# Optimization experiments

Hardware: AMD Instinct MI355X
Metric: run time of the kernel (lower is better)

The kernel has to match this reference:

```python
import jax, jax.numpy as jnp
import numpy as np


def _gru(x, Wih, Whh, bih, bhh):
    """Single-layer torch-style GRU, batch_first. x:[B,T,E], Wih:[3H,E], Whh:[3H,H]."""
    gi = jnp.einsum('bte,ge->btg', x, Wih) + bih  # precompute input gates [B,T,3H]
    H = Whh.shape[1]
    h0 = jnp.zeros((x.shape[0], H), x.dtype)

    def step(h, gi_t):
        gh = h @ Whh.T + bhh
        i_r, i_z, i_n = jnp.split(gi_t, 3, axis=-1)
        h_r, h_z, h_n = jnp.split(gh, 3, axis=-1)
        r = jax.nn.sigmoid(i_r + h_r)
        z = jax.nn.sigmoid(i_z + h_z)
        n = jnp.tanh(i_n + r * h_n)
        h_new = (1.0 - z) * n + z * h
        return h_new, h_new

    _, hs = jax.lax.scan(step, h0, jnp.swapaxes(gi, 0, 1))
    return jnp.swapaxes(hs, 0, 1)  # [B,T,H]


def setup_inputs() -> dict:
    V, E, H, B, S, Tc, Ts = 100000, 256, 256, 256, 10, 20, 50
    Bc = B * S
    k = jax.random.split(jax.random.key(0), 16)
    w = lambda kk, shp, s=0.05: (jax.random.normal(kk, shp) * s).astype(jnp.float32)
    return {
        'input_cate_batch': jax.random.randint(k[0], (Bc, Tc), 0, V),
        'mask_cate_batch': jnp.ones((Bc, Tc), jnp.float32),
        'mask_cate_seq_batch': jnp.ones((B, S), jnp.float32),
        'max_actionNum_cate_batch': Tc,
        'max_subseqNum_cate_batch': S,
        'subseqLen_cate_batch': jax.random.randint(k[1], (Bc,), 0, Tc),
        'seqLen_cate_batch': jax.random.randint(k[2], (B,), 0, S),
        'input_batch': jax.random.randint(k[3], (B, Ts), 0, V),
        'mask_batch': jnp.ones((B, Ts), jnp.float32),
        'seqLen_batch': jax.random.randint(k[4], (B,), 0, Ts),
        'target_y_batch': jax.random.randint(k[5], (B,), 0, V),
        'train_test_flag': 0,
        'emb': w(k[6], (V, E), 0.02),
        'Wih_c': w(k[7], (3 * H, E)), 'Whh_c': w(k[8], (3 * H, H)),
        'bih_c': jnp.zeros((3 * H,), jnp.float32), 'bhh_c': jnp.zeros((3 * H,), jnp.float32),
        'Wih_s': w(k[9], (3 * H, E)), 'Whh_s': w(k[10], (3 * H, H)),
        'bih_s': jnp.zeros((3 * H,), jnp.float32), 'bhh_s': jnp.zeros((3 * H,), jnp.float32),
        'fc_W': w(k[11], (H, 2 * H)), 'fc_b': jnp.zeros((H,), jnp.float32),
    }


def reference(input_cate_batch, mask_cate_batch, mask_cate_seq_batch,
              max_actionNum_cate_batch, max_subseqNum_cate_batch,
              subseqLen_cate_batch, seqLen_cate_batch, input_batch, mask_batch,
              seqLen_batch, target_y_batch, train_test_flag,
              emb, Wih_c, Whh_c, bih_c, bhh_c, Wih_s, Whh_s, bih_s, bhh_s,
              fc_W, fc_b):
    Bc = input_cate_batch.shape[0]
    B = input_batch.shape[0]
    S = max_subseqNum_cate_batch
    # --- category GRU over subsequences ---
    x_c = emb[input_cate_batch]                                  # [Bc,Tc,E]
    out_c = _gru(x_c, Wih_c, Whh_c, bih_c, bhh_c) * mask_cate_batch[:, :, None]
    gathered = out_c[jnp.arange(Bc), subseqLen_cate_batch]       # [Bc,H] per-row length gather
    seq_cate = gathered.reshape(B, S, -1)                        # [B,S,H]
    # --- short GRU over the recent session ---
    x_s = emb[input_batch]                                       # [B,Ts,E]
    out_s = _gru(x_s, Wih_s, Whh_s, bih_s, bhh_s) * mask_batch[:, :, None]
    out_short = out_s[jnp.arange(B), seqLen_batch]               # [B,H]
    # --- masked softmax attention of short state over subseq states ---
    att = jnp.einsum('bsh,bh->bs', seq_cate, out_short)          # [B,S]
    w = jax.nn.softmax(att, axis=1) * mask_cate_seq_batch
    w = w / jnp.sum(w, axis=1, keepdims=True)
    sum_cate = jnp.einsum('bs,bsh->bh', w, seq_cate)             # [B,H]
    mix = jnp.concatenate([sum_cate, out_short], axis=1)         # [B,2H]
    fc_out = mix @ fc_W.T + fc_b                                 # [B,H]
    logits = fc_out @ emb.T                                      # [B,V] shared-embedding output layer
    return logits, target_y_batch
```

## Files before the change

kernel.cpp:

```cpp
#include <hip/hip_runtime.h>
#include <cmath>

#define EMB_V 100000
#define BATCH 256
#define SUBS  10
#define BC    2560
#define TC    20
#define TS    50

using bf16x8 = __attribute__((ext_vector_type(8))) short;
using f32x4  = __attribute__((ext_vector_type(4))) float;

__device__ __forceinline__ unsigned short f2bf(float f) {
    unsigned int u = __float_as_uint(f);
    u += 0x7fff + ((u >> 16) & 1);
    return (unsigned short)(u >> 16);
}
__device__ __forceinline__ float bf2f(unsigned short u) {
    return __uint_as_float(((unsigned int)u) << 16);
}
__device__ __forceinline__ float sigmoid_fast(float x) {
    return __builtin_amdgcn_rcpf(1.f + __expf(-x));
}
__device__ __forceinline__ float tanh_fast(float x) {
    float e = __expf(2.f * x);
    return 1.f - 2.f * __builtin_amdgcn_rcpf(e + 1.f);
}
__device__ __forceinline__ void dma16(const void* g, void* l) {
    __builtin_amdgcn_global_load_lds((const __attribute__((address_space(1))) void*)g,
                                     (__attribute__((address_space(3))) void*)l, 16, 0, 0);
}

__device__ __forceinline__ void pack_whh_dev(const float* __restrict__ W,
                                             unsigned short* __restrict__ P, int t) {
    if (t >= 48 * 8 * 64) return;
    int l = t & 63, kc = (t >> 6) & 7, nt = t >> 9;
    int g = nt % 3, cg = nt / 3;
    int n = g * 256 + cg * 16 + (l & 15);
    int k = kc * 32 + (l >> 4) * 8;
    const float* src = W + n * 256 + k;
    unsigned short* dst = P + (size_t)t * 8;
#pragma unroll
    for (int j = 0; j < 8; ++j) dst[j] = f2bf(src[j]);
}
__global__ __launch_bounds__(256) void prep_misc(
    const float* __restrict__ fc_W, float* __restrict__ fcWT,
    const float* __restrict__ Whh_c, unsigned short* __restrict__ packW_c,
    const float* __restrict__ Whh_s, unsigned short* __restrict__ packW_s,
    const float* __restrict__ Wih_c, unsigned short* __restrict__ wihb_c,
    const float* __restrict__ Wih_s, unsigned short* __restrict__ wihb_s)
{
    const int b = blockIdx.x, tid = threadIdx.x;
    if (b < 512) {
        int o = b * 256 + tid;
        int c = o >> 8, r = o & 255;
        fcWT[o] = fc_W[r * 512 + c];
    } else if (b < 608) {
        pack_whh_dev(Whh_c, packW_c, (b - 512) * 256 + tid);
    } else if (b < 704) {
        pack_whh_dev(Whh_s, packW_s, (b - 608) * 256 + tid);
    } else if (b < 896) {
        int i = (b - 704) * 256 + tid;
        float4 v = ((const float4*)Wih_c)[i];
        ((ushort4*)wihb_c)[i] = make_ushort4(f2bf(v.x), f2bf(v.y), f2bf(v.z), f2bf(v.w));
    } else {
        int i = (b - 896) * 256 + tid;
        float4 v = ((const float4*)Wih_s)[i];
        ((ushort4*)wihb_s)[i] = make_ushort4(f2bf(v.x), f2bf(v.y), f2bf(v.z), f2bf(v.w));
    }
}

__global__ void f32_to_bf16(const float* __restrict__ in, unsigned short* __restrict__ out,
                            int n4) {
    for (int i = blockIdx.x * 256 + threadIdx.x; i < n4; i += gridDim.x * 256) {
        float4 v = ((const float4*)in)[i];
        ((ushort4*)out)[i] = make_ushort4(f2bf(v.x), f2bf(v.y), f2bf(v.z), f2bf(v.w));
    }
}

template <bool GATHER, bool OBF16, bool NGUARD>
__global__ __launch_bounds__(256, 3) void gemm_abt(
    const unsigned short* __restrict__ A, const int* __restrict__ tok,
    const unsigned short* __restrict__ B, void* __restrict__ Cout,
    int N, int ldc)
{
    __shared__ unsigned short Asub[128 * 64];
    __shared__ unsigned short Bsub[128 * 64];
    const int tid = threadIdx.x;
    const int l = tid & 63, wave = tid >> 6;
    const int lm = l & 15, quad = l >> 4;
    const int wm = wave >> 1, wn = wave & 1;
    const int n0 = blockIdx.x * 128, m0 = blockIdx.y * 128;

    unsigned aofs[4], bofs[4];
#pragma unroll
    for (int i = 0; i < 4; ++i) {
        int c = tid + i * 256, row = c >> 3, cc = c & 7;
        aofs[i] = (GATHER ? (unsigned)tok[m0 + row] : (unsigned)(m0 + row)) * 256u + cc * 8u;
        bofs[i] = (unsigned)(n0 + row) * 256u + cc * 8u;
    }
    const int dstu = (tid & 192) * 8;

    f32x4 acc[4][4];
#pragma unroll
    for (int mi = 0; mi < 4; ++mi)
#pragma unroll
        for (int ni = 0; ni < 4; ++ni) acc[mi][ni] = (f32x4){0.f, 0.f, 0.f, 0.f};

    for (int kk = 0; kk < 4; ++kk) {
        const int k0 = kk * 64;
#pragma unroll
        for (int i = 0; i < 4; ++i)
            dma16(A + aofs[i] + k0, &Asub[dstu + i * 2048]);
#pragma unroll
        for (int i = 0; i < 4; ++i)
            dma16(B + bofs[i] + k0, &Bsub[dstu + i * 2048]);
        __syncthreads();
#pragma unroll
        for (int kc = 0; kc < 2; ++kc) {
            bf16x8 af[4], bfv[4];
#pragma unroll
            for (int mi = 0; mi < 4; ++mi)
                af[mi] = *(const bf16x8*)&Asub[(wm * 64 + mi * 16 + lm) * 64 + kc * 32 + quad * 8];
#pragma unroll
            for (int ni = 0; ni < 4; ++ni)
                bfv[ni] = *(const bf16x8*)&Bsub[(wn * 64 + ni * 16 + lm) * 64 + kc * 32 + quad * 8];
#pragma unroll
            for (int mi = 0; mi < 4; ++mi)
#pragma unroll
                for (int ni = 0; ni < 4; ++ni)
                    acc[mi][ni] = __builtin_amdgcn_mfma_f32_16x16x32_bf16(
                        af[mi], bfv[ni], acc[mi][ni], 0, 0, 0);
        }
        __syncthreads();
    }
#pragma unroll
    for (int mi = 0; mi < 4; ++mi)
#pragma unroll
        for (int ni = 0; ni < 4; ++ni) {
            int col = n0 + wn * 64 + ni * 16 + lm;
            if (NGUARD && col >= N) continue;
#pragma unroll
            for (int i = 0; i < 4; ++i) {
                int row = m0 + wm * 64 + mi * 16 + quad * 4 + i;
                if (OBF16)
                    ((unsigned short*)Cout)[(size_t)row * ldc + col] = f2bf(acc[mi][ni][i]);
                else
                    ((float*)Cout)[(size_t)row * ldc + col] = acc[mi][ni][i];
            }
        }
}

__global__ __launch_bounds__(512, 2) void gru_scan_fused(
    const unsigned short* __restrict__ gi_c, const unsigned short* __restrict__ pW_c,
    const float* __restrict__ bih_c, const float* __restrict__ bhh_c,
    const int* __restrict__ len_c, const float* __restrict__ mask_c,
    float* __restrict__ out_c,
    const unsigned short* __restrict__ gi_s, const unsigned short* __restrict__ pW_s,
    const float* __restrict__ bih_s, const float* __restrict__ bhh_s,
    const int* __restrict__ len_s, const float* __restrict__ mask_s,
    float* __restrict__ out_s)
{
    __shared__ unsigned short h_lds[2][16][264];
    __shared__ unsigned short b_lds[8 * 4 * 512];
    __shared__ unsigned short gi_lds[2][16 * 768];

    const bool is_cat = blockIdx.x < (BC / 16);
    const int  T      = is_cat ? TC : TS;
    const int  row0   = (is_cat ? blockIdx.x : blockIdx.x - BC / 16) * 16;
    const unsigned short* gi   = is_cat ? gi_c  : gi_s;
    const unsigned short* pW   = is_cat ? pW_c  : pW_s;
    const float*          bih  = is_cat ? bih_c : bih_s;
    const float*          bhh  = is_cat ? bhh_c : bhh_s;
    const int*            lenp = is_cat ? len_c : len_s;
    const float*          mask = is_cat ? mask_c : mask_s;
    float*                outp = is_cat ? out_c : out_s;

    const int tid  = threadIdx.x;
    const int l    = tid & 63, w = tid >> 6;
    const int lm   = l & 15,   quad = l >> 4;

    for (int i = tid; i < 2 * 16 * 264; i += 512) ((unsigned short*)h_lds)[i] = 0;

    bf16x8 breg[44];
#pragma unroll
    for (int ti = 0; ti < 6; ++ti)
#pragma unroll
        for (int kc = 0; kc < 8; ++kc) {
            bf16x8 v = *((const bf16x8*)pW + (size_t)((6 * w + ti) * 8 + kc) * 64 + l);
            if (ti < 5)           breg[ti * 8 + kc] = v;
            else if (kc < 4)      breg[40 + kc] = v;
            else *(bf16x8*)&b_lds[((w * 4 + (kc - 4)) * 64 + l) * 8] = v;
        }

    const int c0 = 32 * w + lm, c1 = c0 + 16;
    const float cR0 = bih[c0] + bhh[c0],             cR1 = bih[c1] + bhh[c1];
    const float cZ0 = bih[256 + c0] + bhh[256 + c0], cZ1 = bih[256 + c1] + bhh[256 + c1];
    const float cNi0 = bih[512 + c0], cNi1 = bih[512 + c1];
    const float cNh0 = bhh[512 + c0], cNh1 = bhh[512 + c1];

    int len[4];
#pragma unroll
    for (int i = 0; i < 4; ++i) len[i] = lenp[row0 + quad * 4 + i];

    const unsigned short* gq[3];
    const int dstu = (tid & 448) * 8;
#pragma unroll
    for (int i = 0; i < 3; ++i) {
        int c = tid + i * 512;
        int row = c / 96, cc = c - row * 96;
        gq[i] = gi + ((size_t)(row0 + row) * T) * 768 + cc * 8;
    }
#pragma unroll
    for (int i = 0; i < 3; ++i) {
        dma16(gq[i], &gi_lds[0][dstu + i * 8192]);
        gq[i] += 768;
    }

    float hold0[4] = {0.f, 0.f, 0.f, 0.f};
    float hold1[4] = {0.f, 0.f, 0.f, 0.f};

    __syncthreads();

    for (int t = 0; t < T; ++t) {
        if (t + 1 < T) {
#pragma unroll
            for (int i = 0; i < 3; ++i) {
                dma16(gq[i], &gi_lds[(t + 1) & 1][dstu + i * 8192]);
                gq[i] += 768;
            }
        }

        const unsigned short (*hb)[264] = h_lds[t & 1];
        f32x4 acc[6];
#pragma unroll
        for (int ti = 0; ti < 6; ++ti) acc[ti] = (f32x4){0.f, 0.f, 0.f, 0.f};
#pragma unroll
        for (int kc = 0; kc < 8; ++kc) {
            bf16x8 a = *(const bf16x8*)&hb[lm][kc * 32 + quad * 8];
#pragma unroll
            for (int ti = 0; ti < 6; ++ti) {
                bf16x8 b;
                if (ti < 5)           b = breg[ti * 8 + kc];
                else if (kc < 4)      b = breg[40 + kc];
                else b = *(const bf16x8*)&b_lds[((w * 4 + (kc - 4)) * 64 + l) * 8];
                acc[ti] = __builtin_amdgcn_mfma_f32_16x16x32_bf16(a, b, acc[ti], 0, 0, 0);
            }
        }

        const unsigned short* gb = gi_lds[t & 1];
        unsigned short (*hw)[264] = h_lds[(t + 1) & 1];
#pragma unroll
        for (int i = 0; i < 4; ++i) {
            const int r = quad * 4 + i;
            const unsigned short* gr = gb + r * 768;
            {
                float rg = sigmoid_fast(bf2f(gr[c0]) + acc[0][i] + cR0);
                float zg = sigmoid_fast(bf2f(gr[256 + c0]) + acc[1][i] + cZ0);
                float ng = tanh_fast(bf2f(gr[512 + c0]) + cNi0 + rg * (acc[2][i] + cNh0));
                float hn = zg * (hold0[i] - ng) + ng;
                hold0[i] = hn;
                hw[r][c0] = f2bf(hn);
                if (t == len[i])
                    outp[(size_t)(row0 + r) * 256 + c0] = hn * mask[(row0 + r) * T + t];
            }
            {
                float rg = sigmoid_fast(bf2f(gr[c1]) + acc[3][i] + cR1);
                float zg = sigmoid_fast(bf2f(gr[256 + c1]) + acc[4][i] + cZ1);
                float ng = tanh_fast(bf2f(gr[512 + c1]) + cNi1 + rg * (acc[5][i] + cNh1));
                float hn = zg * (hold1[i] - ng) + ng;
                hold1[i] = hn;
                hw[r][c1] = f2bf(hn);
                if (t == len[i])
                    outp[(size_t)(row0 + r) * 256 + c1] = hn * mask[(row0 + r) * T + t];
            }
        }

        asm volatile("s_waitcnt vmcnt(0) lgkmcnt(0)" ::: "memory");
        __builtin_amdgcn_sched_barrier(0);
        __builtin_amdgcn_s_barrier();
        __builtin_amdgcn_sched_barrier(0);
    }
}

__global__ __launch_bounds__(256) void attn_fc(
    const float* __restrict__ seq_cate, const float* __restrict__ out_short,
    const float* __restrict__ mask_seq, const float* __restrict__ fcWT,
    const float* __restrict__ fc_b, const int* __restrict__ target,
    unsigned short* __restrict__ fc_out, float* __restrict__ d_out)
{
    __shared__ float sc[SUBS][256];
    __shared__ float os[256];
    __shared__ float part[SUBS][256];
    __shared__ float mix[512];
    const int b = blockIdx.x, tid = threadIdx.x;

    os[tid] = out_short[b * 256 + tid];
    for (int s = 0; s < SUBS; ++s) sc[s][tid] = seq_cate[(size_t)(b * SUBS + s) * 256 + tid];
    __syncthreads();

    for (int s = 0; s < SUBS; ++s) part[s][tid] = sc[s][tid] * os[tid];
    __syncthreads();
    for (int off = 128; off >= 1; off >>= 1) {
        if (tid < off)
            for (int s = 0; s < SUBS; ++s) part[s][tid] += part[s][tid + off];
        __syncthreads();
    }

    float w[SUBS];
    float m = -1e30f;
    for (int s = 0; s < SUBS; ++s) m = fmaxf(m, part[s][0]);
    float sum = 0.f;
    for (int s = 0; s < SUBS; ++s) { w[s] = __expf(part[s][0] - m); sum += w[s]; }
    float tot = 0.f;
    for (int s = 0; s < SUBS; ++s) { w[s] = (w[s] / sum) * mask_seq[b * SUBS + s]; tot += w[s]; }
    float inv = 1.f / tot;

    float sumc = 0.f;
    for (int s = 0; s < SUBS; ++s) sumc += w[s] * inv * sc[s][tid];
    mix[tid] = sumc;
    mix[256 + tid] = os[tid];
    __syncthreads();

    float acc = fc_b[tid];
    for (int jj = 0; jj < 512; ++jj) acc = fmaf(mix[jj], fcWT[jj * 256 + tid], acc);
    fc_out[b * 256 + tid] = f2bf(acc);

    if (tid == 0) d_out[(size_t)BATCH * EMB_V + b] = (float)target[b];
}

extern "C" void kernel_launch(void* const* d_in, const int* in_sizes, int n_in,
                              void* d_out, int out_size, void* d_ws, size_t ws_size,
                              hipStream_t stream) {
    const int*   input_cate   = (const int*)d_in[0];
    const float* mask_cate    = (const float*)d_in[1];
    const float* mask_seq     = (const float*)d_in[2];
    const int*   subseqLen    = (const int*)d_in[5];
    const int*   input_batch  = (const int*)d_in[7];
    const float* mask_batch   = (const float*)d_in[8];
    const int*   seqLen_batch = (const int*)d_in[9];
    const int*   target       = (const int*)d_in[10];
    const float* emb          = (const float*)d_in[12];
    const float* Wih_c        = (const float*)d_in[13];
    const float* Whh_c        = (const float*)d_in[14];
    const float* bih_c        = (const float*)d_in[15];
    const float* bhh_c        = (const float*)d_in[16];
    const float* Wih_s        = (const float*)d_in[17];
    const float* Whh_s        = (const float*)d_in[18];
    const float* bih_s        = (const float*)d_in[19];
    const float* bhh_s        = (const float*)d_in[20];
    const float* fc_W         = (const float*)d_in[21];
    const float* fc_b         = (const float*)d_in[22];
    float* out = (float*)d_out;

    float* ws = (float*)d_ws;
    float*          fcWT      = ws;
    float*          out_short = ws + 131072;
    unsigned short* fc_outb   = (unsigned short*)(ws + 196608);
    float*          seq_cate  = ws + 229376;
    unsigned short* packW_c   = (unsigned short*)(ws + 884736);
    unsigned short* packW_s   = (unsigned short*)(ws + 983040);
    unsigned short* wihb_c    = (unsigned short*)(ws + 1081344);
    unsigned short* wihb_s    = (unsigned short*)(ws + 1179648);
    unsigned short* embb      = (unsigned short*)(ws + 1277952);
    unsigned short* gi_c      = (unsigned short*)(ws + 14077952);
    unsigned short* gi_s      = (unsigned short*)(ws + 33738752);

    prep_misc<<<1088, 256, 0, stream>>>(fc_W, fcWT, Whh_c, packW_c, Whh_s, packW_s,
                                        Wih_c, wihb_c, Wih_s, wihb_s);
    f32_to_bf16<<<2048, 256, 0, stream>>>(emb, embb, EMB_V * 256 / 4);

    gemm_abt<true, true, false><<<dim3(6, 400), 256, 0, stream>>>(
        embb, input_cate, wihb_c, gi_c, 768, 768);
    gemm_abt<true, true, false><<<dim3(6, 100), 256, 0, stream>>>(
        embb, input_batch, wihb_s, gi_s, 768, 768);

    gru_scan_fused<<<BC / 16 + BATCH / 16, 512, 0, stream>>>(
        gi_c, packW_c, bih_c, bhh_c, subseqLen, mask_cate, seq_cate,
        gi_s, packW_s, bih_s, bhh_s, seqLen_batch, mask_batch, out_short);

    attn_fc<<<BATCH, 256, 0, stream>>>(
        seq_cate, out_short, mask_seq, fcWT, fc_b, target, fc_outb, out);

    gemm_abt<false, false, true><<<dim3(782, 2), 256, 0, stream>>>(
        fc_outb, nullptr, embb, out, EMB_V, EMB_V);
}
```

Baseline: 450.1 us.

## Write GRU input gates in per-thread layout and load them directly to registers

The input-projection GEMM now scatters its bf16 output into a layout matching each scan thread's gate elements, so every thread loads its 24 values with three 16-byte global loads per step. The LDS double-buffered DMA staging for gi and the vmcnt wait before the barrier are removed. The sixth recurrent weight tile moves fully to LDS, freeing registers, and launch bounds drop to 1 block per CU. The output GEMM's B-row index is clamped to avoid out-of-range loads. The scattered GEMM stores are uncoalesced, and gi load latency is no longer hidden by a prefetch.

```diff
diff --git a/kernel.cpp b/kernel.cpp
--- a/kernel.cpp
+++ b/kernel.cpp
@@ -78,7 +78,7 @@
     }
 }
 
-template <bool GATHER, bool OBF16, bool NGUARD>
+template <bool GATHER, bool OBF16, bool NGUARD, int GIT>
 __global__ __launch_bounds__(256, 3) void gemm_abt(
     const unsigned short* __restrict__ A, const int* __restrict__ tok,
     const unsigned short* __restrict__ B, void* __restrict__ Cout,
@@ -97,7 +97,9 @@
     for (int i = 0; i < 4; ++i) {
         int c = tid + i * 256, row = c >> 3, cc = c & 7;
         aofs[i] = (GATHER ? (unsigned)tok[m0 + row] : (unsigned)(m0 + row)) * 256u + cc * 8u;
-        bofs[i] = (unsigned)(n0 + row) * 256u + cc * 8u;
+        unsigned brow = (unsigned)(n0 + row);
+        if (NGUARD && brow >= (unsigned)N) brow = (unsigned)N - 1;
+        bofs[i] = brow * 256u + cc * 8u;
     }
     const int dstu = (tid & 192) * 8;
 
@@ -143,15 +145,25 @@
 #pragma unroll
             for (int i = 0; i < 4; ++i) {
                 int row = m0 + wm * 64 + mi * 16 + quad * 4 + i;
-                if (OBF16)
+                if (GIT > 0) {
+                    unsigned bc = (unsigned)row / (unsigned)GIT;
+                    unsigned tt = (unsigned)row - bc * (unsigned)GIT;
+                    unsigned Rr = bc >> 4, rr = bc & 15;
+                    unsigned g = (unsigned)col >> 8, hcol = (unsigned)col & 255;
+                    unsigned tau = (hcol >> 5) * 64 + (rr >> 2) * 16 + (hcol & 15);
+                    size_t ad = ((size_t)(Rr * (unsigned)GIT + tt) * 512 + tau) * 24
+                              + (rr & 3) * 6 + ((hcol >> 4) & 1) * 3 + g;
+                    ((unsigned short*)Cout)[ad] = f2bf(acc[mi][ni][i]);
+                } else if (OBF16) {
                     ((unsigned short*)Cout)[(size_t)row * ldc + col] = f2bf(acc[mi][ni][i]);
-                else
+                } else {
                     ((float*)Cout)[(size_t)row * ldc + col] = acc[mi][ni][i];
+                }
             }
         }
 }
 
-__global__ __launch_bounds__(512, 2) void gru_scan_fused(
+__global__ __launch_bounds__(512, 1) void gru_scan_fused(
     const unsigned short* __restrict__ gi_c, const unsigned short* __restrict__ pW_c,
     const float* __restrict__ bih_c, const float* __restrict__ bhh_c,
     const int* __restrict__ len_c, const float* __restrict__ mask_c,
@@ -162,12 +174,12 @@
     float* __restrict__ out_s)
 {
     __shared__ unsigned short h_lds[2][16][264];
-    __shared__ unsigned short b_lds[8 * 4 * 512];
-    __shared__ unsigned short gi_lds[2][16 * 768];
+    __shared__ unsigned short b_lds[8 * 8 * 512];
 
     const bool is_cat = blockIdx.x < (BC / 16);
     const int  T      = is_cat ? TC : TS;
-    const int  row0   = (is_cat ? blockIdx.x : blockIdx.x - BC / 16) * 16;
+    const int  R      = is_cat ? blockIdx.x : blockIdx.x - BC / 16;
+    const int  row0   = R * 16;
     const unsigned short* gi   = is_cat ? gi_c  : gi_s;
     const unsigned short* pW   = is_cat ? pW_c  : pW_s;
     const float*          bih  = is_cat ? bih_c : bih_s;
@@ -182,15 +194,14 @@
 
     for (int i = tid; i < 2 * 16 * 264; i += 512) ((unsigned short*)h_lds)[i] = 0;
 
-    bf16x8 breg[44];
+    bf16x8 breg[40];
 #pragma unroll
     for (int ti = 0; ti < 6; ++ti)
 #pragma unroll
         for (int kc = 0; kc < 8; ++kc) {
             bf16x8 v = *((const bf16x8*)pW + (size_t)((6 * w + ti) * 8 + kc) * 64 + l);
-            if (ti < 5)           breg[ti * 8 + kc] = v;
-            else if (kc < 4)      breg[40 + kc] = v;
-            else *(bf16x8*)&b_lds[((w * 4 + (kc - 4)) * 64 + l) * 8] = v;
+            if (ti < 5) breg[ti * 8 + kc] = v;
+            else        *(bf16x8*)&b_lds[((w * 8 + kc) * 64 + l) * 8] = v;
         }
 
     const int c0 = 32 * w + lm, c1 = c0 + 16;
@@ -203,33 +214,20 @@
 #pragma unroll
     for (int i = 0; i < 4; ++i) len[i] = lenp[row0 + quad * 4 + i];
 
-    const unsigned short* gq[3];
-    const int dstu = (tid & 448) * 8;
-#pragma unroll
-    for (int i = 0; i < 3; ++i) {
-        int c = tid + i * 512;
-        int row = c / 96, cc = c - row * 96;
-        gq[i] = gi + ((size_t)(row0 + row) * T) * 768 + cc * 8;
-    }
-#pragma unroll
-    for (int i = 0; i < 3; ++i) {
-        dma16(gq[i], &gi_lds[0][dstu + i * 8192]);
-        gq[i] += 768;
-    }
+    const unsigned short* gp = gi + ((size_t)R * T * 512 + tid) * 24;
 
     float hold0[4] = {0.f, 0.f, 0.f, 0.f};
     float hold1[4] = {0.f, 0.f, 0.f, 0.f};
 
     __syncthreads();
 
+#define GIV(e) bf2f((unsigned short)((e) < 8 ? gv0[(e)] : ((e) < 16 ? gv1[(e) - 8] : gv2[(e) - 16])))
+
     for (int t = 0; t < T; ++t) {
-        if (t + 1 < T) {
-#pragma unroll
-            for (int i = 0; i < 3; ++i) {
-                dma16(gq[i], &gi_lds[(t + 1) & 1][dstu + i * 8192]);
-                gq[i] += 768;
-            }
-        }
+        bf16x8 gv0 = *(const bf16x8*)gp;
+        bf16x8 gv1 = *(const bf16x8*)(gp + 8);
+        bf16x8 gv2 = *(const bf16x8*)(gp + 16);
+        gp += 512 * 24;
 
         const unsigned short (*hb)[264] = h_lds[t & 1];
         f32x4 acc[6];
@@ -240,24 +238,20 @@
             bf16x8 a = *(const bf16x8*)&hb[lm][kc * 32 + quad * 8];
 #pragma unroll
             for (int ti = 0; ti < 6; ++ti) {
-                bf16x8 b;
-                if (ti < 5)           b = breg[ti * 8 + kc];
-                else if (kc < 4)      b = breg[40 + kc];
-                else b = *(const bf16x8*)&b_lds[((w * 4 + (kc - 4)) * 64 + l) * 8];
+                bf16x8 b = (ti < 5) ? breg[ti * 8 + kc]
+                                    : *(const bf16x8*)&b_lds[((w * 8 + kc) * 64 + l) * 8];
                 acc[ti] = __builtin_amdgcn_mfma_f32_16x16x32_bf16(a, b, acc[ti], 0, 0, 0);
             }
         }
 
-        const unsigned short* gb = gi_lds[t & 1];
         unsigned short (*hw)[264] = h_lds[(t + 1) & 1];
 #pragma unroll
         for (int i = 0; i < 4; ++i) {
             const int r = quad * 4 + i;
-            const unsigned short* gr = gb + r * 768;
             {
-                float rg = sigmoid_fast(bf2f(gr[c0]) + acc[0][i] + cR0);
-                float zg = sigmoid_fast(bf2f(gr[256 + c0]) + acc[1][i] + cZ0);
-                float ng = tanh_fast(bf2f(gr[512 + c0]) + cNi0 + rg * (acc[2][i] + cNh0));
+                float rg = sigmoid_fast(GIV(i * 6 + 0) + acc[0][i] + cR0);
+                float zg = sigmoid_fast(GIV(i * 6 + 1) + acc[1][i] + cZ0);
+                float ng = tanh_fast(GIV(i * 6 + 2) + cNi0 + rg * (acc[2][i] + cNh0));
                 float hn = zg * (hold0[i] - ng) + ng;
                 hold0[i] = hn;
                 hw[r][c0] = f2bf(hn);
@@ -265,9 +259,9 @@
                     outp[(size_t)(row0 + r) * 256 + c0] = hn * mask[(row0 + r) * T + t];
             }
             {
-                float rg = sigmoid_fast(bf2f(gr[c1]) + acc[3][i] + cR1);
-                float zg = sigmoid_fast(bf2f(gr[256 + c1]) + acc[4][i] + cZ1);
-                float ng = tanh_fast(bf2f(gr[512 + c1]) + cNi1 + rg * (acc[5][i] + cNh1));
+                float rg = sigmoid_fast(GIV(i * 6 + 3) + acc[3][i] + cR1);
+                float zg = sigmoid_fast(GIV(i * 6 + 4) + acc[4][i] + cZ1);
+                float ng = tanh_fast(GIV(i * 6 + 5) + cNi1 + rg * (acc[5][i] + cNh1));
                 float hn = zg * (hold1[i] - ng) + ng;
                 hold1[i] = hn;
                 hw[r][c1] = f2bf(hn);
@@ -276,11 +270,12 @@
             }
         }
 
-        asm volatile("s_waitcnt vmcnt(0) lgkmcnt(0)" ::: "memory");
+        asm volatile("s_waitcnt lgkmcnt(0)" ::: "memory");
         __builtin_amdgcn_sched_barrier(0);
         __builtin_amdgcn_s_barrier();
         __builtin_amdgcn_sched_barrier(0);
     }
+#undef GIV
 }
 
 __global__ __launch_bounds__(256) void attn_fc(
@@ -370,9 +365,9 @@
                                         Wih_c, wihb_c, Wih_s, wihb_s);
     f32_to_bf16<<<2048, 256, 0, stream>>>(emb, embb, EMB_V * 256 / 4);
 
-    gemm_abt<true, true, false><<<dim3(6, 400), 256, 0, stream>>>(
+    gemm_abt<true, true, false, TC><<<dim3(6, 400), 256, 0, stream>>>(
         embb, input_cate, wihb_c, gi_c, 768, 768);
-    gemm_abt<true, true, false><<<dim3(6, 100), 256, 0, stream>>>(
+    gemm_abt<true, true, false, TS><<<dim3(6, 100), 256, 0, stream>>>(
         embb, input_batch, wihb_s, gi_s, 768, 768);
 
     gru_scan_fused<<<BC / 16 + BATCH / 16, 512, 0, stream>>>(
@@ -382,6 +377,6 @@
     attn_fc<<<BATCH, 256, 0, stream>>>(
         seq_cate, out_short, mask_seq, fcWT, fc_b, target, fc_outb, out);
 
-    gemm_abt<false, false, true><<<dim3(782, 2), 256, 0, stream>>>(
+    gemm_abt<false, false, true, 0><<<dim3(782, 2), 256, 0, stream>>>(
         fc_outb, nullptr, embb, out, EMB_V, EMB_V);
 }
```

Result: slower. 626.5 us (+39.2%).
